# Kernel optimization log

Measured on AMD Instinct MI355X. Metric: run time of the kernel, lower is better.

Reference implementation:

```python
import jax, jax.numpy as jnp
import numpy as np

W_CUB = 0.1
W_CD = 1.0
W_EXT = 0.01
W_SPS = 0.01
THRED = 24.0
COS_EPS = 1e-4

# cube face buffers (6 faces x 3 coords)
MASK_PROJECT = jnp.array([[0,1,1],[0,1,1],[1,0,1],[1,0,1],[1,1,0],[1,1,0]], jnp.float32)
MASK_PLANE   = jnp.array([[1,0,0],[1,0,0],[0,1,0],[0,1,0],[0,0,1],[0,0,1]], jnp.float32)
CUBE_NORMAL  = jnp.array([[-1,0,0],[1,0,0],[0,-1,0],[0,1,0],[0,0,-1],[0,0,1]], jnp.float32)
# torch repeat(...,3,...) of [[-1,-1,-1],[1,1,1]] tiles it -> [c0,c1,c0,c1,c0,c1]
CUBE_PLANES6 = jnp.tile(jnp.array([[-1.,-1.,-1.],[1.,1.,1.]], jnp.float32), (3,1))


def setup_inputs():
    B, P, N, S = 4, 24, 3072, 128
    key = jax.random.key(0)
    ks = jax.random.split(key, 8)
    pc_inver = jax.random.normal(ks[0], (B, P, N, 3), jnp.float32)
    normals_inver = jax.random.normal(ks[1], (B, P, N, 3), jnp.float32)
    scale = jax.random.uniform(ks[2], (B, P, 3), jnp.float32) * 0.9 + 0.1
    shape = jax.random.uniform(ks[3], (B, P, 2), jnp.float32) * 1.3 + 0.2
    exist = jax.random.uniform(ks[4], (B, P, 1), jnp.float32) * 0.98 + 0.01
    assign_matrix = jax.nn.softmax(jax.random.normal(ks[5], (B, N, P), jnp.float32), axis=-1)
    etas = jax.random.uniform(ks[6], (B, P, S), jnp.float32, minval=-jnp.pi/2, maxval=jnp.pi/2)
    omegas = jax.random.uniform(ks[7], (B, P, S), jnp.float32, minval=-jnp.pi, maxval=jnp.pi)
    return dict(pc_inver=pc_inver, normals_inver=normals_inver, scale=scale,
                shape=shape, exist=exist, assign_matrix=assign_matrix,
                etas=etas, omegas=omegas)


def _fexp(x, p):
    return jnp.sign(x) * jnp.abs(x) ** p


def _sample_sq_points(scale, eps, etas, omegas):
    # scale (B,P,3), eps (B,P,2), etas/omegas (B,P,S) -> (B,P,S,3)
    etas = jnp.where(etas == 0, 1e-6, etas)
    omegas = jnp.where(omegas == 0, 1e-6, omegas)
    a1, a2, a3 = scale[..., 0:1], scale[..., 1:2], scale[..., 2:3]
    e1, e2 = eps[..., 0:1], eps[..., 1:2]
    ce, se = jnp.cos(etas), jnp.sin(etas)
    co, so = jnp.cos(omegas), jnp.sin(omegas)
    x = a1 * _fexp(ce, e1) * _fexp(co, e2)
    y = a2 * _fexp(ce, e1) * _fexp(so, e2)
    z = a3 * _fexp(se, e1)
    fix = lambda v: (jnp.where(v > 0, 1.0, -1.0)) * jnp.maximum(jnp.abs(v), 1e-6)
    return jnp.stack([fix(x), fix(y), fix(z)], -1)


def _cd_loss(pc_inver, scale, shape, exist, assign_matrix, etas, omegas):
    X = _sample_sq_points(scale, shape, etas, omegas)          # (B,P,S,3)
    diff = X[:, :, :, None, :] - pc_inver[:, :, None, :, :]    # (B,P,S,N,3)
    D = jnp.sum(diff * diff, -1)                               # (B,P,S,N)
    pcl2prim = jnp.min(D, axis=2)                              # (B,P,N)
    pcl_loss = jnp.mean(jnp.sum(jnp.swapaxes(pcl2prim, 1, 2) * assign_matrix, -1))
    prim2pcl = jnp.mean(jnp.min(D, axis=3), axis=-1)           # (B,P)
    e = exist[..., 0]
    prim_loss = jnp.mean(jnp.sum(prim2pcl * e, -1) / (jnp.sum(e, -1) + 1e-6))
    return pcl_loss, prim_loss


def _cuboid_loss(pc_inver, normals_inver, scale, assign_matrix):
    pc = jnp.swapaxes(pc_inver, 1, 2)        # (B,N,P,3)
    nrm = jnp.swapaxes(normals_inver, 1, 2)  # (B,N,P,3)
    n_norm = jnp.maximum(jnp.linalg.norm(nrm, axis=-1, keepdims=True), COS_EPS)
    cos = jnp.einsum('bnpc,fc->bnpf', nrm, CUBE_NORMAL) / n_norm  # ||cube_normal||=1
    idx = jnp.argmax(cos, axis=-1)           # (B,N,P)
    s = scale[:, None, :, None, :]           # (B,1,P,1,3)
    proj = pc[:, :, :, None, :] * MASK_PROJECT + (CUBE_PLANES6 * s) * MASK_PLANE  # (B,N,P,6,3)
    proj = jnp.clip(proj, -s, s)
    proj_sel = jnp.take_along_axis(proj, idx[..., None, None], axis=3)[..., 0, :]  # (B,N,P,3)
    d = jnp.sum((proj_sel - pc) ** 2, -1)    # (B,N,P)
    return jnp.mean(jnp.sum(d * assign_matrix, -1))


def _common_losses(assign_matrix, exist):
    gt = jax.lax.stop_gradient((jnp.sum(assign_matrix, 1) > THRED).astype(jnp.float32))  # (B,P)
    p = exist[..., 0]
    bce = -jnp.mean(gt * jnp.log(p) + (1.0 - gt) * jnp.log1p(-p))
    N = assign_matrix.shape[1]
    sps = jnp.mean(jnp.mean(jnp.sqrt(jnp.sum(assign_matrix, 1) / N + 0.01), -1) ** 2)
    return bce, sps


def reference(pc_inver, normals_inver, scale, shape, exist, assign_matrix, etas, omegas):
    cub = _cuboid_loss(pc_inver, normals_inver, scale, assign_matrix)
    pcl_loss, prim_loss = _cd_loss(pc_inver, scale, shape, exist, assign_matrix, etas, omegas)
    bce, sps = _common_losses(assign_matrix, exist)
    return W_CUB * cub + W_CD * (pcl_loss + prim_loss) + W_EXT * bce + W_SPS * sps
```

## Files before the change

### kernel.cpp

```cpp
#include <hip/hip_runtime.h>
#include <math.h>

#define BB 4
#define PP 24
#define NN 3072
#define SS 128
#define NSPLIT 12
#define CHUNK 256

#define WS_X      0
#define WS_PART   49152
#define PART_STRIDE 132
#define WS_BP     201216

__device__ __forceinline__ float fexp_f(float v, float p) {
    float m = powf(fabsf(v), p);
    float s = (v > 0.f) ? 1.f : ((v < 0.f) ? -1.f : 0.f);
    return s * m;
}
__device__ __forceinline__ float fix_f(float v) {
    return ((v > 0.f) ? 1.f : -1.f) * fmaxf(fabsf(v), 1e-6f);
}
__device__ __forceinline__ float wave_sum(float v) {
    #pragma unroll
    for (int off = 32; off > 0; off >>= 1) v += __shfl_down(v, off);
    return v;
}

__global__ __launch_bounds__(128) void superdec_sample(
    const float* __restrict__ scale, const float* __restrict__ shape,
    const float* __restrict__ etas, const float* __restrict__ omegas,
    float* __restrict__ ws)
{
    const int bp = blockIdx.x;
    const int s  = threadIdx.x;
    const float a1 = scale[bp * 3 + 0];
    const float a2 = scale[bp * 3 + 1];
    const float a3 = scale[bp * 3 + 2];
    const float e1 = shape[bp * 2 + 0];
    const float e2 = shape[bp * 2 + 1];
    float eta = etas[bp * SS + s];
    float omg = omegas[bp * SS + s];
    eta = (eta == 0.f) ? 1e-6f : eta;
    omg = (omg == 0.f) ? 1e-6f : omg;
    float ce = cosf(eta), se = sinf(eta);
    float co = cosf(omg), so = sinf(omg);
    float fce = fexp_f(ce, e1);
    float x = a1 * fce * fexp_f(co, e2);
    float y = a2 * fce * fexp_f(so, e2);
    float z = a3 * fexp_f(se, e1);
    float4* X = (float4*)(ws + WS_X);
    X[bp * SS + s] = make_float4(fix_f(x), fix_f(y), fix_f(z), 0.f);
}

__global__ __launch_bounds__(256) void superdec_main(
    const float* __restrict__ pc, const float* __restrict__ nrm,
    const float* __restrict__ scale, const float* __restrict__ assign,
    float* __restrict__ ws)
{
    const int blk   = blockIdx.x;
    const int bp    = blk / NSPLIT;
    const int split = blk % NSPLIT;
    const int b     = bp / PP;
    const int p     = bp % PP;
    const int tid   = threadIdx.x;
    const int n0    = split * CHUNK;

    __shared__ float4 Xs[SS];
    __shared__ float4 Pts[CHUNK];
    __shared__ float  red[CHUNK];
    __shared__ float  wsum[12];

    const float sc0 = scale[bp * 3 + 0];
    const float sc1 = scale[bp * 3 + 1];
    const float sc2 = scale[bp * 3 + 2];

    const float4* Xg = (const float4*)(ws + WS_X);
    if (tid < SS) Xs[tid] = Xg[bp * SS + tid];

    const float* pcb = pc + ((size_t)bp * NN + n0) * 3;
    const float px = pcb[tid * 3 + 0];
    const float py = pcb[tid * 3 + 1];
    const float pz = pcb[tid * 3 + 2];
    Pts[tid] = make_float4(px, py, pz, 0.f);
    __syncthreads();

    float m0 = 3.4e38f, m1 = 3.4e38f, m2 = 3.4e38f, m3 = 3.4e38f;
    #pragma unroll 4
    for (int s = 0; s < SS; s += 4) {
        float4 x0 = Xs[s + 0];
        float4 x1 = Xs[s + 1];
        float4 x2 = Xs[s + 2];
        float4 x3 = Xs[s + 3];
        float dx, dy, dz, d;
        dx = x0.x - px; dy = x0.y - py; dz = x0.z - pz;
        d = fmaf(dx, dx, fmaf(dy, dy, dz * dz)); m0 = fminf(m0, d);
        dx = x1.x - px; dy = x1.y - py; dz = x1.z - pz;
        d = fmaf(dx, dx, fmaf(dy, dy, dz * dz)); m1 = fminf(m1, d);
        dx = x2.x - px; dy = x2.y - py; dz = x2.z - pz;
        d = fmaf(dx, dx, fmaf(dy, dy, dz * dz)); m2 = fminf(m2, d);
        dx = x3.x - px; dy = x3.y - py; dz = x3.z - pz;
        d = fmaf(dx, dx, fmaf(dy, dy, dz * dz)); m3 = fminf(m3, d);
    }
    const float dmin = fminf(fminf(m0, m1), fminf(m2, m3));
    const float am = assign[((size_t)b * NN + n0 + tid) * PP + p];
    float acc_pcl = dmin * am;

    const float* nrb = nrm + ((size_t)bp * NN + n0) * 3;
    const float nx = nrb[tid * 3 + 0];
    const float ny = nrb[tid * 3 + 1];
    const float nz = nrb[tid * 3 + 2];
    float best = -nx; int idx = 0;
    if ( nx > best) { best =  nx; idx = 1; }
    if (-ny > best) { best = -ny; idx = 2; }
    if ( ny > best) { best =  ny; idx = 3; }
    if (-nz > best) { best = -nz; idx = 4; }
    if ( nz > best) { best =  nz; idx = 5; }
    const int c = idx >> 1;
    const float scc = (c == 0) ? sc0 : ((c == 1) ? sc1 : sc2);
    const float fv  = (idx & 1) ? scc : -scc;
    float pr0 = (c == 0) ? fv : fminf(fmaxf(px, -sc0), sc0);
    float pr1 = (c == 1) ? fv : fminf(fmaxf(py, -sc1), sc1);
    float pr2 = (c == 2) ? fv : fminf(fmaxf(pz, -sc2), sc2);
    float d0 = pr0 - px, d1 = pr1 - py, d2 = pr2 - pz;
    float acc_cub = fmaf(d0, d0, fmaf(d1, d1, d2 * d2)) * am;

    {
        float s0 = wave_sum(acc_pcl);
        float s1 = wave_sum(acc_cub);
        float s2 = wave_sum(am);
        const int lane = tid & 63, wave = tid >> 6;
        if (lane == 0) {
            wsum[wave * 3 + 0] = s0;
            wsum[wave * 3 + 1] = s1;
            wsum[wave * 3 + 2] = s2;
        }
    }
    __syncthreads();

    {
        const int s    = tid & (SS - 1);
        const int half = tid >> 7;
        const float4 xv = Xs[s];
        const int nb0 = half * (CHUNK / 2);
        float b0 = 3.4e38f, b1 = 3.4e38f;
        #pragma unroll 4
        for (int n = 0; n < CHUNK / 2; n += 2) {
            float4 p0 = Pts[nb0 + n];
            float4 p1 = Pts[nb0 + n + 1];
            float dx, dy, dz, d;
            dx = xv.x - p0.x; dy = xv.y - p0.y; dz = xv.z - p0.z;
            d = fmaf(dx, dx, fmaf(dy, dy, dz * dz)); b0 = fminf(b0, d);
            dx = xv.x - p1.x; dy = xv.y - p1.y; dz = xv.z - p1.z;
            d = fmaf(dx, dx, fmaf(dy, dy, dz * dz)); b1 = fminf(b1, d);
        }
        red[tid] = fminf(b0, b1);
    }
    __syncthreads();

    float* part = ws + WS_PART + (size_t)(bp * NSPLIT + split) * PART_STRIDE;
    if (tid < SS) part[tid] = fminf(red[tid], red[tid + SS]);
    if (tid == 0) {
        part[SS + 0] = wsum[0] + wsum[3] + wsum[6] + wsum[9];
        part[SS + 1] = wsum[1] + wsum[4] + wsum[7] + wsum[10];
        part[SS + 2] = wsum[2] + wsum[5] + wsum[8] + wsum[11];
    }
}

__global__ __launch_bounds__(128) void superdec_reduce(
    const float* __restrict__ ws_in, float* __restrict__ ws_out)
{
    const int bp  = blockIdx.x;
    const int tid = threadIdx.x;
    __shared__ float sh[8];

    const float* base = ws_in + WS_PART + (size_t)bp * NSPLIT * PART_STRIDE;
    float m = 3.4e38f;
    #pragma unroll
    for (int sp = 0; sp < NSPLIT; ++sp)
        m = fminf(m, base[sp * PART_STRIDE + tid]);

    float s = wave_sum(m);
    const int lane = tid & 63, wave = tid >> 6;
    if (lane == 0) sh[wave] = s;
    if (tid < 3) {
        float acc = 0.f;
        #pragma unroll
        for (int sp = 0; sp < NSPLIT; ++sp)
            acc += base[sp * PART_STRIDE + SS + tid];
        sh[4 + tid] = acc;
    }
    __syncthreads();
    if (tid == 0) {
        float* o = ws_out + WS_BP + bp * 4;
        o[0] = sh[4];
        o[1] = sh[5];
        o[2] = sh[6];
        o[3] = (sh[0] + sh[1]) / (float)SS;
    }
}

__global__ __launch_bounds__(128) void superdec_final(
    const float* __restrict__ ws, const float* __restrict__ exist,
    float* __restrict__ out)
{
    __shared__ float s_pcl[96], s_cub[96], s_pe[96], s_e[96], s_bce[96], s_sq[96];
    const int t = threadIdx.x;
    if (t < BB * PP) {
        const float* o = ws + WS_BP + t * 4;
        float pclv = o[0], cubv = o[1], colsum = o[2], prim = o[3];
        float e = exist[t];
        float gt = (colsum > 24.0f) ? 1.f : 0.f;
        s_pcl[t] = pclv;
        s_cub[t] = cubv;
        s_pe[t]  = prim * e;
        s_e[t]   = e;
        s_bce[t] = gt * logf(e) + (1.f - gt) * log1pf(-e);
        s_sq[t]  = sqrtf(colsum / (float)NN + 0.01f);
    }
    __syncthreads();
    if (t == 0) {
        float pcl_sum = 0.f, cub_sum = 0.f, bce_sum = 0.f;
        for (int i = 0; i < BB * PP; ++i) {
            pcl_sum += s_pcl[i]; cub_sum += s_cub[i]; bce_sum += s_bce[i];
        }
        float prim_loss = 0.f, sps = 0.f;
        for (int b = 0; b < BB; ++b) {
            float pe = 0.f, ee = 0.f, sq = 0.f;
            for (int p = 0; p < PP; ++p) {
                int i = b * PP + p;
                pe += s_pe[i]; ee += s_e[i]; sq += s_sq[i];
            }
            prim_loss += pe / (ee + 1e-6f);
            float mb = sq / (float)PP;
            sps += mb * mb;
        }
        prim_loss /= (float)BB;
        sps       /= (float)BB;
        float pcl_loss = pcl_sum / (float)(BB * NN);
        float cub      = cub_sum / (float)(BB * NN);
        float bce      = -bce_sum / (float)(BB * PP);
        out[0] = 0.1f * cub + 1.0f * (pcl_loss + prim_loss) + 0.01f * bce + 0.01f * sps;
    }
}

extern "C" void kernel_launch(void* const* d_in, const int* in_sizes, int n_in,
                              void* d_out, int out_size, void* d_ws, size_t ws_size,
                              hipStream_t stream) {
    const float* pc     = (const float*)d_in[0];
    const float* nrm    = (const float*)d_in[1];
    const float* scale  = (const float*)d_in[2];
    const float* shape  = (const float*)d_in[3];
    const float* exist  = (const float*)d_in[4];
    const float* assign = (const float*)d_in[5];
    const float* etas   = (const float*)d_in[6];
    const float* omegas = (const float*)d_in[7];
    float* ws  = (float*)d_ws;
    float* out = (float*)d_out;

    superdec_sample<<<BB * PP, SS, 0, stream>>>(scale, shape, etas, omegas, ws);
    superdec_main<<<BB * PP * NSPLIT, CHUNK, 0, stream>>>(pc, nrm, scale, assign, ws);
    superdec_reduce<<<BB * PP, SS, 0, stream>>>(ws, ws);
    superdec_final<<<1, 128, 0, stream>>>(ws, exist, out);
}
```

Before: 101.5 us.

## Fuse sampling into main kernel, expand distances algebraically, merge reduce kernels

Superquadric point sampling moves into the main kernel, so each of the 6 splits per primitive recomputes it. The separate reduce and final kernels become a single 1024-thread kernel, cutting four launches to two. Squared distances are rewritten as -2x·p + |x|^2 + |p|^2, which saves arithmetic in both Chamfer directions but can lose precision through cancellation. Each thread now handles two points with a larger chunk and fewer blocks, which improves reuse but lowers parallelism.

```diff
diff --git a/kernel.cpp b/kernel.cpp
--- a/kernel.cpp
+++ b/kernel.cpp
@@ -5,13 +5,9 @@
 #define PP 24
 #define NN 3072
 #define SS 128
-#define NSPLIT 12
-#define CHUNK 256
-
-#define WS_X      0
-#define WS_PART   49152
+#define CHUNK 512
+#define NSPLIT 6
 #define PART_STRIDE 132
-#define WS_BP     201216
 
 __device__ __forceinline__ float fexp_f(float v, float p) {
     float m = powf(fabsf(v), p);
@@ -26,90 +22,9 @@
     for (int off = 32; off > 0; off >>= 1) v += __shfl_down(v, off);
     return v;
 }
-
-__global__ __launch_bounds__(128) void superdec_sample(
-    const float* __restrict__ scale, const float* __restrict__ shape,
-    const float* __restrict__ etas, const float* __restrict__ omegas,
-    float* __restrict__ ws)
-{
-    const int bp = blockIdx.x;
-    const int s  = threadIdx.x;
-    const float a1 = scale[bp * 3 + 0];
-    const float a2 = scale[bp * 3 + 1];
-    const float a3 = scale[bp * 3 + 2];
-    const float e1 = shape[bp * 2 + 0];
-    const float e2 = shape[bp * 2 + 1];
-    float eta = etas[bp * SS + s];
-    float omg = omegas[bp * SS + s];
-    eta = (eta == 0.f) ? 1e-6f : eta;
-    omg = (omg == 0.f) ? 1e-6f : omg;
-    float ce = cosf(eta), se = sinf(eta);
-    float co = cosf(omg), so = sinf(omg);
-    float fce = fexp_f(ce, e1);
-    float x = a1 * fce * fexp_f(co, e2);
-    float y = a2 * fce * fexp_f(so, e2);
-    float z = a3 * fexp_f(se, e1);
-    float4* X = (float4*)(ws + WS_X);
-    X[bp * SS + s] = make_float4(fix_f(x), fix_f(y), fix_f(z), 0.f);
-}
-
-__global__ __launch_bounds__(256) void superdec_main(
-    const float* __restrict__ pc, const float* __restrict__ nrm,
-    const float* __restrict__ scale, const float* __restrict__ assign,
-    float* __restrict__ ws)
-{
-    const int blk   = blockIdx.x;
-    const int bp    = blk / NSPLIT;
-    const int split = blk % NSPLIT;
-    const int b     = bp / PP;
-    const int p     = bp % PP;
-    const int tid   = threadIdx.x;
-    const int n0    = split * CHUNK;
-
-    __shared__ float4 Xs[SS];
-    __shared__ float4 Pts[CHUNK];
-    __shared__ float  red[CHUNK];
-    __shared__ float  wsum[12];
-
-    const float sc0 = scale[bp * 3 + 0];
-    const float sc1 = scale[bp * 3 + 1];
-    const float sc2 = scale[bp * 3 + 2];
-
-    const float4* Xg = (const float4*)(ws + WS_X);
-    if (tid < SS) Xs[tid] = Xg[bp * SS + tid];
-
-    const float* pcb = pc + ((size_t)bp * NN + n0) * 3;
-    const float px = pcb[tid * 3 + 0];
-    const float py = pcb[tid * 3 + 1];
-    const float pz = pcb[tid * 3 + 2];
-    Pts[tid] = make_float4(px, py, pz, 0.f);
-    __syncthreads();
-
-    float m0 = 3.4e38f, m1 = 3.4e38f, m2 = 3.4e38f, m3 = 3.4e38f;
-    #pragma unroll 4
-    for (int s = 0; s < SS; s += 4) {
-        float4 x0 = Xs[s + 0];
-        float4 x1 = Xs[s + 1];
-        float4 x2 = Xs[s + 2];
-        float4 x3 = Xs[s + 3];
-        float dx, dy, dz, d;
-        dx = x0.x - px; dy = x0.y - py; dz = x0.z - pz;
-        d = fmaf(dx, dx, fmaf(dy, dy, dz * dz)); m0 = fminf(m0, d);
-        dx = x1.x - px; dy = x1.y - py; dz = x1.z - pz;
-        d = fmaf(dx, dx, fmaf(dy, dy, dz * dz)); m1 = fminf(m1, d);
-        dx = x2.x - px; dy = x2.y - py; dz = x2.z - pz;
-        d = fmaf(dx, dx, fmaf(dy, dy, dz * dz)); m2 = fminf(m2, d);
-        dx = x3.x - px; dy = x3.y - py; dz = x3.z - pz;
-        d = fmaf(dx, dx, fmaf(dy, dy, dz * dz)); m3 = fminf(m3, d);
-    }
-    const float dmin = fminf(fminf(m0, m1), fminf(m2, m3));
-    const float am = assign[((size_t)b * NN + n0 + tid) * PP + p];
-    float acc_pcl = dmin * am;
-
-    const float* nrb = nrm + ((size_t)bp * NN + n0) * 3;
-    const float nx = nrb[tid * 3 + 0];
-    const float ny = nrb[tid * 3 + 1];
-    const float nz = nrb[tid * 3 + 2];
+__device__ __forceinline__ float cub_dist(float px, float py, float pz,
+                                          float nx, float ny, float nz,
+                                          float sc0, float sc1, float sc2) {
     float best = -nx; int idx = 0;
     if ( nx > best) { best =  nx; idx = 1; }
     if (-ny > best) { best = -ny; idx = 2; }
@@ -123,12 +38,87 @@
     float pr1 = (c == 1) ? fv : fminf(fmaxf(py, -sc1), sc1);
     float pr2 = (c == 2) ? fv : fminf(fmaxf(pz, -sc2), sc2);
     float d0 = pr0 - px, d1 = pr1 - py, d2 = pr2 - pz;
-    float acc_cub = fmaf(d0, d0, fmaf(d1, d1, d2 * d2)) * am;
+    return fmaf(d0, d0, fmaf(d1, d1, d2 * d2));
+}
+
+__global__ __launch_bounds__(256) void superdec_main(
+    const float* __restrict__ pc, const float* __restrict__ nrm,
+    const float* __restrict__ scale, const float* __restrict__ shape,
+    const float* __restrict__ assign,
+    const float* __restrict__ etas, const float* __restrict__ omegas,
+    float* __restrict__ ws)
+{
+    const int blk   = blockIdx.x;
+    const int bp    = blk / NSPLIT;
+    const int split = blk % NSPLIT;
+    const int b     = bp / PP;
+    const int p     = bp % PP;
+    const int tid   = threadIdx.x;
+    const int n0    = split * CHUNK;
+
+    __shared__ float4 Xs[SS];
+    __shared__ float4 Pts[CHUNK];
+    __shared__ float  red[CHUNK];
+    __shared__ float  wsum[12];
+
+    const float sc0 = scale[bp * 3 + 0];
+    const float sc1 = scale[bp * 3 + 1];
+    const float sc2 = scale[bp * 3 + 2];
+
+    if (tid < SS) {
+        const float e1 = shape[bp * 2 + 0];
+        const float e2 = shape[bp * 2 + 1];
+        float eta = etas[bp * SS + tid];
+        float omg = omegas[bp * SS + tid];
+        eta = (eta == 0.f) ? 1e-6f : eta;
+        omg = (omg == 0.f) ? 1e-6f : omg;
+        float ce = cosf(eta), se = sinf(eta);
+        float co = cosf(omg), so = sinf(omg);
+        float fce = fexp_f(ce, e1);
+        float x = fix_f(sc0 * fce * fexp_f(co, e2));
+        float y = fix_f(sc1 * fce * fexp_f(so, e2));
+        float z = fix_f(sc2 * fexp_f(se, e1));
+        float xsq = fmaf(x, x, fmaf(y, y, z * z));
+        Xs[tid] = make_float4(-2.f * x, -2.f * y, -2.f * z, xsq);
+    }
+
+    const float* pcb = pc  + ((size_t)bp * NN + n0) * 3;
+    const float* nrb = nrm + ((size_t)bp * NN + n0) * 3;
+    const int iA = tid, iB = tid + 256;
+    const float pxA = pcb[iA * 3 + 0], pyA = pcb[iA * 3 + 1], pzA = pcb[iA * 3 + 2];
+    const float pxB = pcb[iB * 3 + 0], pyB = pcb[iB * 3 + 1], pzB = pcb[iB * 3 + 2];
+    const float psqA = fmaf(pxA, pxA, fmaf(pyA, pyA, pzA * pzA));
+    const float psqB = fmaf(pxB, pxB, fmaf(pyB, pyB, pzB * pzB));
+    Pts[iA] = make_float4(pxA, pyA, pzA, psqA);
+    Pts[iB] = make_float4(pxB, pyB, pzB, psqB);
+    const float amA = assign[((size_t)b * NN + n0 + iA) * PP + p];
+    const float amB = assign[((size_t)b * NN + n0 + iB) * PP + p];
+    const float nxA = nrb[iA * 3 + 0], nyA = nrb[iA * 3 + 1], nzA = nrb[iA * 3 + 2];
+    const float nxB = nrb[iB * 3 + 0], nyB = nrb[iB * 3 + 1], nzB = nrb[iB * 3 + 2];
+    __syncthreads();
+
+    float mA0 = 3.4e38f, mA1 = 3.4e38f, mB0 = 3.4e38f, mB1 = 3.4e38f;
+    #pragma unroll 4
+    for (int s = 0; s < SS; s += 2) {
+        float4 x0 = Xs[s + 0];
+        float4 x1 = Xs[s + 1];
+        float d;
+        d = fmaf(x0.x, pxA, fmaf(x0.y, pyA, fmaf(x0.z, pzA, x0.w))); mA0 = fminf(mA0, d);
+        d = fmaf(x1.x, pxA, fmaf(x1.y, pyA, fmaf(x1.z, pzA, x1.w))); mA1 = fminf(mA1, d);
+        d = fmaf(x0.x, pxB, fmaf(x0.y, pyB, fmaf(x0.z, pzB, x0.w))); mB0 = fminf(mB0, d);
+        d = fmaf(x1.x, pxB, fmaf(x1.y, pyB, fmaf(x1.z, pzB, x1.w))); mB1 = fminf(mB1, d);
+    }
+    const float dminA = fminf(mA0, mA1) + psqA;
+    const float dminB = fminf(mB0, mB1) + psqB;
+    float acc_pcl = dminA * amA + dminB * amB;
+    float acc_cub = cub_dist(pxA, pyA, pzA, nxA, nyA, nzA, sc0, sc1, sc2) * amA
+                  + cub_dist(pxB, pyB, pzB, nxB, nyB, nzB, sc0, sc1, sc2) * amB;
+    float acc_am  = amA + amB;
 
     {
         float s0 = wave_sum(acc_pcl);
         float s1 = wave_sum(acc_cub);
-        float s2 = wave_sum(am);
+        float s2 = wave_sum(acc_am);
         const int lane = tid & 63, wave = tid >> 6;
         if (lane == 0) {
             wsum[wave * 3 + 0] = s0;
@@ -136,30 +126,35 @@
             wsum[wave * 3 + 2] = s2;
         }
     }
-    __syncthreads();
 
     {
-        const int s    = tid & (SS - 1);
-        const int half = tid >> 7;
-        const float4 xv = Xs[s];
-        const int nb0 = half * (CHUNK / 2);
-        float b0 = 3.4e38f, b1 = 3.4e38f;
+        const int sA = tid & 63;
+        const int q  = tid >> 6;
+        const float4 xa = Xs[sA];
+        const float4 xb = Xs[sA + 64];
+        const int nb0 = q * (CHUNK / 4);
+        float ma0 = 3.4e38f, ma1 = 3.4e38f, mb0 = 3.4e38f, mb1 = 3.4e38f;
         #pragma unroll 4
-        for (int n = 0; n < CHUNK / 2; n += 2) {
+        for (int n = 0; n < CHUNK / 4; n += 2) {
             float4 p0 = Pts[nb0 + n];
             float4 p1 = Pts[nb0 + n + 1];
-            float dx, dy, dz, d;
-            dx = xv.x - p0.x; dy = xv.y - p0.y; dz = xv.z - p0.z;
-            d = fmaf(dx, dx, fmaf(dy, dy, dz * dz)); b0 = fminf(b0, d);
-            dx = xv.x - p1.x; dy = xv.y - p1.y; dz = xv.z - p1.z;
-            d = fmaf(dx, dx, fmaf(dy, dy, dz * dz)); b1 = fminf(b1, d);
+            float d;
+            d = fmaf(xa.x, p0.x, fmaf(xa.y, p0.y, fmaf(xa.z, p0.z, p0.w))); ma0 = fminf(ma0, d);
+            d = fmaf(xa.x, p1.x, fmaf(xa.y, p1.y, fmaf(xa.z, p1.z, p1.w))); ma1 = fminf(ma1, d);
+            d = fmaf(xb.x, p0.x, fmaf(xb.y, p0.y, fmaf(xb.z, p0.z, p0.w))); mb0 = fminf(mb0, d);
+            d = fmaf(xb.x, p1.x, fmaf(xb.y, p1.y, fmaf(xb.z, p1.z, p1.w))); mb1 = fminf(mb1, d);
         }
-        red[tid] = fminf(b0, b1);
-    }
-    __syncthreads();
-
-    float* part = ws + WS_PART + (size_t)(bp * NSPLIT + split) * PART_STRIDE;
-    if (tid < SS) part[tid] = fminf(red[tid], red[tid + SS]);
+        red[q * 128 + sA]      = fminf(ma0, ma1);
+        red[q * 128 + 64 + sA] = fminf(mb0, mb1);
+    }
+    __syncthreads();
+
+    float* part = ws + (size_t)(bp * NSPLIT + split) * PART_STRIDE;
+    if (tid < SS) {
+        float m = fminf(fminf(red[tid], red[128 + tid]),
+                        fminf(red[256 + tid], red[384 + tid]));
+        part[tid] = m + Xs[tid].w;
+    }
     if (tid == 0) {
         part[SS + 0] = wsum[0] + wsum[3] + wsum[6] + wsum[9];
         part[SS + 1] = wsum[1] + wsum[4] + wsum[7] + wsum[10];
@@ -167,69 +162,55 @@
     }
 }
 
-__global__ __launch_bounds__(128) void superdec_reduce(
-    const float* __restrict__ ws_in, float* __restrict__ ws_out)
-{
-    const int bp  = blockIdx.x;
-    const int tid = threadIdx.x;
-    __shared__ float sh[8];
-
-    const float* base = ws_in + WS_PART + (size_t)bp * NSPLIT * PART_STRIDE;
-    float m = 3.4e38f;
-    #pragma unroll
-    for (int sp = 0; sp < NSPLIT; ++sp)
-        m = fminf(m, base[sp * PART_STRIDE + tid]);
-
-    float s = wave_sum(m);
-    const int lane = tid & 63, wave = tid >> 6;
-    if (lane == 0) sh[wave] = s;
-    if (tid < 3) {
-        float acc = 0.f;
-        #pragma unroll
-        for (int sp = 0; sp < NSPLIT; ++sp)
-            acc += base[sp * PART_STRIDE + SS + tid];
-        sh[4 + tid] = acc;
-    }
-    __syncthreads();
-    if (tid == 0) {
-        float* o = ws_out + WS_BP + bp * 4;
-        o[0] = sh[4];
-        o[1] = sh[5];
-        o[2] = sh[6];
-        o[3] = (sh[0] + sh[1]) / (float)SS;
-    }
-}
-
-__global__ __launch_bounds__(128) void superdec_final(
+__global__ __launch_bounds__(1024) void superdec_reduce_final(
     const float* __restrict__ ws, const float* __restrict__ exist,
     float* __restrict__ out)
 {
-    __shared__ float s_pcl[96], s_cub[96], s_pe[96], s_e[96], s_bce[96], s_sq[96];
-    const int t = threadIdx.x;
-    if (t < BB * PP) {
-        const float* o = ws + WS_BP + t * 4;
-        float pclv = o[0], cubv = o[1], colsum = o[2], prim = o[3];
-        float e = exist[t];
-        float gt = (colsum > 24.0f) ? 1.f : 0.f;
-        s_pcl[t] = pclv;
-        s_cub[t] = cubv;
-        s_pe[t]  = prim * e;
-        s_e[t]   = e;
-        s_bce[t] = gt * logf(e) + (1.f - gt) * log1pf(-e);
-        s_sq[t]  = sqrtf(colsum / (float)NN + 0.01f);
-    }
-    __syncthreads();
+    __shared__ float s_prim[96], s_pcl[96], s_cub[96], s_sum[96];
+    const int t    = threadIdx.x;
+    const int lane = t & 63;
+    if (t < 96) s_prim[t] = 0.f;
+    __syncthreads();
+
+    #pragma unroll
+    for (int k = 0; k < (96 * 128) / 1024; ++k) {
+        const int idx = t + k * 1024;
+        const int bp  = idx >> 7;
+        const int s   = idx & 127;
+        const float* base = ws + (size_t)bp * (NSPLIT * PART_STRIDE) + s;
+        float m = fminf(fminf(fminf(base[0 * PART_STRIDE], base[1 * PART_STRIDE]),
+                              fminf(base[2 * PART_STRIDE], base[3 * PART_STRIDE])),
+                        fminf(base[4 * PART_STRIDE], base[5 * PART_STRIDE]));
+        float sm = wave_sum(m);
+        if (lane == 0) atomicAdd(&s_prim[bp], sm);
+    }
+    if (t < 96 * 3) {
+        const int bp = t / 3, v = t % 3;
+        const float* base = ws + (size_t)bp * (NSPLIT * PART_STRIDE) + SS + v;
+        float acc = 0.f;
+        #pragma unroll
+        for (int sp = 0; sp < NSPLIT; ++sp) acc += base[sp * PART_STRIDE];
+        if      (v == 0) s_pcl[bp] = acc;
+        else if (v == 1) s_cub[bp] = acc;
+        else             s_sum[bp] = acc;
+    }
+    __syncthreads();
+
     if (t == 0) {
-        float pcl_sum = 0.f, cub_sum = 0.f, bce_sum = 0.f;
-        for (int i = 0; i < BB * PP; ++i) {
-            pcl_sum += s_pcl[i]; cub_sum += s_cub[i]; bce_sum += s_bce[i];
-        }
-        float prim_loss = 0.f, sps = 0.f;
-        for (int b = 0; b < BB; ++b) {
+        float pcl_sum = 0.f, cub_sum = 0.f, bce_sum = 0.f, prim_loss = 0.f, sps = 0.f;
+        for (int b_ = 0; b_ < BB; ++b_) {
             float pe = 0.f, ee = 0.f, sq = 0.f;
-            for (int p = 0; p < PP; ++p) {
-                int i = b * PP + p;
-                pe += s_pe[i]; ee += s_e[i]; sq += s_sq[i];
+            for (int p_ = 0; p_ < PP; ++p_) {
+                const int i = b_ * PP + p_;
+                const float colsum = s_sum[i];
+                const float e = exist[i];
+                const float gt = (colsum > 24.0f) ? 1.f : 0.f;
+                pcl_sum += s_pcl[i];
+                cub_sum += s_cub[i];
+                bce_sum += gt * logf(e) + (1.f - gt) * log1pf(-e);
+                pe += (s_prim[i] / (float)SS) * e;
+                ee += e;
+                sq += sqrtf(colsum / (float)NN + 0.01f);
             }
             prim_loss += pe / (ee + 1e-6f);
             float mb = sq / (float)PP;
@@ -258,8 +239,7 @@
     float* ws  = (float*)d_ws;
     float* out = (float*)d_out;
 
-    superdec_sample<<<BB * PP, SS, 0, stream>>>(scale, shape, etas, omegas, ws);
-    superdec_main<<<BB * PP * NSPLIT, CHUNK, 0, stream>>>(pc, nrm, scale, assign, ws);
-    superdec_reduce<<<BB * PP, SS, 0, stream>>>(ws, ws);
-    superdec_final<<<1, 128, 0, stream>>>(ws, exist, out);
-}
+    superdec_main<<<BB * PP * NSPLIT, 256, 0, stream>>>(
+        pc, nrm, scale, shape, assign, etas, omegas, ws);
+    superdec_reduce_final<<<1, 1024, 0, stream>>>(ws, exist, out);
+}
```

Measured after the change: 132.6 us. +30.6%, slower.
